# Optimization experiments

Measured on AMD Instinct MI355X. Metric: run time of the kernel, lower is better.

## Reference

```python
import jax, jax.numpy as jnp
import numpy as np

B, T, I, H, L = 64, 512, 512, 512, 2

def _xavier(key, shape):
    fan_in, fan_out = shape
    limit = float(np.sqrt(6.0 / (fan_in + fan_out)))
    return jax.random.uniform(key, shape, jnp.float32, -limit, limit)

def setup_inputs() -> dict:
    key = jax.random.key(0)
    ks = jax.random.split(key, 16)
    x = jax.random.normal(ks[0], (B, T, I), jnp.float32)
    h = jax.random.normal(ks[1], (L, B, H), jnp.float32)
    c = jax.random.normal(ks[2], (L, B, H), jnp.float32)
    # Gate order: i, f, g, o (concatenated along output dim -> [*, 4H])
    W_x0 = jnp.concatenate([_xavier(ks[3 + j], (I, H)) for j in range(4)], axis=1)
    W_h0 = jnp.concatenate([_xavier(ks[7 + j], (H, H)) for j in range(4)], axis=1)
    W_x1 = jnp.concatenate([_xavier(ks[11], (H, H)), _xavier(ks[12], (H, H)),
                            _xavier(ks[13], (H, H)), _xavier(ks[14], (H, H))], axis=1)
    W_h1 = jnp.concatenate([jax.random.split(ks[15], 4)[j] is None or _xavier(jax.random.split(ks[15], 4)[j], (H, H)) for j in range(4)], axis=1)
    # 8 scalar biases per layer: (b_ii, b_hi, b_if, b_hf, b_ig, b_hg, b_io, b_ho); zero-init as in torch
    b0 = jnp.zeros((8,), jnp.float32)
    b1 = jnp.zeros((8,), jnp.float32)
    return {"x": x, "h": h, "c": c, "W_x0": W_x0, "W_h0": W_h0, "b0": b0,
            "W_x1": W_x1, "W_h1": W_h1, "b1": b1}

def _lstm_layer(xs, h0, c0, Wx, Wh, b):
    # xs: [B, T, D]; Wx: [D, 4H]; Wh: [H, 4H]; b: [8] scalars
    bg = b[0::2] + b[1::2]  # combined per-gate scalar biases [4]: i, f, g, o
    x_proj = jnp.einsum('btd,dk->btk', xs, Wx)  # precompute input GEMM: [B, T, 4H]

    def step(carry, xp_t):
        h, c = carry
        z = xp_t + h @ Wh  # [B, 4H]
        zi, zf, zg, zo = jnp.split(z, 4, axis=1)
        i = jax.nn.sigmoid(zi + bg[0])
        f = jax.nn.sigmoid(zf + bg[1])
        g = jnp.tanh(zg + bg[2])
        o = jax.nn.sigmoid(zo + bg[3])
        c_new = f * c + i * g
        h_new = o * jnp.tanh(c_new)
        return (h_new, c_new), h_new

    (hT, cT), ys = jax.lax.scan(step, (h0, c0), jnp.swapaxes(x_proj, 0, 1))
    return jnp.swapaxes(ys, 0, 1), hT, cT  # output [B, T, H]

def reference(x, h, c, W_x0, W_h0, b0, W_x1, W_h1, b1):
    out0, h0T, c0T = _lstm_layer(x, h[0], c[0], W_x0, W_h0, b0)
    out1, h1T, c1T = _lstm_layer(out0, h[1], c[1], W_x1, W_h1, b1)
    new_h = jnp.stack([h0T, h1T])  # [L, B, H]
    new_c = jnp.stack([c0T, c1T])
    return out1, new_h, new_c
```

## Files before the change

kernel.cpp:

```cpp
#include <hip/hip_runtime.h>
#include <hip/hip_bf16.h>

#define B_   64
#define T_   512
#define I_   512
#define H_   512
#define NTHR 256

typedef short bf16x8 __attribute__((ext_vector_type(8)));
typedef float f32x4  __attribute__((ext_vector_type(4)));
typedef unsigned long long u64;
typedef unsigned short u16;

#define MFMA(a, b, c) __builtin_amdgcn_mfma_f32_16x16x32_bf16((a), (b), (c), 0, 0, 0)

__device__ __forceinline__ u16 f2b(float f) {
    __hip_bfloat16 h = __float2bfloat16(f);
    return __builtin_bit_cast(u16, h);
}

__device__ __forceinline__ u64 coh_ld64(const void* p) {
    return __hip_atomic_load((const u64*)p, __ATOMIC_RELAXED, __HIP_MEMORY_SCOPE_AGENT);
}
__device__ __forceinline__ void coh_st64(void* p, u64 v) {
    __hip_atomic_store((u64*)p, v, __ATOMIC_RELAXED, __HIP_MEMORY_SCOPE_AGENT);
}
__device__ __forceinline__ bool flag_ge(const int* f, int idx, int tgt) {
    return __hip_atomic_load(f + idx, __ATOMIC_RELAXED, __HIP_MEMORY_SCOPE_AGENT) >= tgt;
}

__device__ __forceinline__ int sc0_ld_i32(const int* p) {
    int v;
    asm volatile("global_load_dword %0, %1, off sc0\n\ts_waitcnt vmcnt(0)"
                 : "=&v"(v) : "v"(p) : "memory");
    return v;
}
__device__ __forceinline__ void sc0_st_i32(int* p, int v) {
    asm volatile("global_store_dword %0, %1, off sc0" :: "v"(p), "v"(v) : "memory");
}

#define GLD16(O, A)                                                         \
  asm volatile(                                                             \
    "global_load_dwordx4 %0, %16, off sc0\n\t"                              \
    "global_load_dwordx4 %1, %16, off offset:64 sc0\n\t"                    \
    "global_load_dwordx4 %2, %16, off offset:128 sc0\n\t"                   \
    "global_load_dwordx4 %3, %16, off offset:192 sc0\n\t"                   \
    "global_load_dwordx4 %4, %16, off offset:256 sc0\n\t"                   \
    "global_load_dwordx4 %5, %16, off offset:320 sc0\n\t"                   \
    "global_load_dwordx4 %6, %16, off offset:384 sc0\n\t"                   \
    "global_load_dwordx4 %7, %16, off offset:448 sc0\n\t"                   \
    "global_load_dwordx4 %8, %16, off offset:512 sc0\n\t"                   \
    "global_load_dwordx4 %9, %16, off offset:576 sc0\n\t"                   \
    "global_load_dwordx4 %10, %16, off offset:640 sc0\n\t"                  \
    "global_load_dwordx4 %11, %16, off offset:704 sc0\n\t"                  \
    "global_load_dwordx4 %12, %16, off offset:768 sc0\n\t"                  \
    "global_load_dwordx4 %13, %16, off offset:832 sc0\n\t"                  \
    "global_load_dwordx4 %14, %16, off offset:896 sc0\n\t"                  \
    "global_load_dwordx4 %15, %16, off offset:960 sc0\n\t"                  \
    "s_waitcnt vmcnt(0)"                                                    \
    : "=&v"(O[0]), "=&v"(O[1]), "=&v"(O[2]), "=&v"(O[3]),                   \
      "=&v"(O[4]), "=&v"(O[5]), "=&v"(O[6]), "=&v"(O[7]),                   \
      "=&v"(O[8]), "=&v"(O[9]), "=&v"(O[10]), "=&v"(O[11]),                 \
      "=&v"(O[12]), "=&v"(O[13]), "=&v"(O[14]), "=&v"(O[15])                \
    : "v"(A) : "memory")

__device__ __forceinline__ void pub_local(u16* ring, int* fp, int fval,
                                          const u16* sca, int lane, int U0) {
    const int r0 = lane >> 3, s0 = lane & 7;
    const int r1 = 8 + r0;
    u64 q0 = *(const u64*)(sca + r0 * 36 + s0 * 4);
    u64 q1 = *(const u64*)(sca + r1 * 36 + s0 * 4);
    u16* d0 = ring + r0 * 512 + U0 + s0 * 4;
    u16* d1 = ring + r1 * 512 + U0 + s0 * 4;
    asm volatile(
        "global_store_dwordx2 %0, %2, off sc0\n\t"
        "global_store_dwordx2 %1, %3, off sc0\n\t"
        "s_waitcnt vmcnt(0)"
        :: "v"(d0), "v"(d1), "v"(q0), "v"(q1) : "memory");
    if (lane == 0) sc0_st_i32(fp, fval);
}

__device__ __forceinline__ void pub_agent(u16* ring, int* fp, int fval,
                                          const u16* sca, int lane, int R0, int U0) {
    const int r0 = lane >> 3, s0 = lane & 7;
    const int r1 = 8 + r0;
    u64 q0 = *(const u64*)(sca + r0 * 36 + s0 * 4);
    u64 q1 = *(const u64*)(sca + r1 * 36 + s0 * 4);
    coh_st64(ring + (size_t)(R0 + r0) * 512 + U0 + s0 * 4, q0);
    coh_st64(ring + (size_t)(R0 + r1) * 512 + U0 + s0 * 4, q1);
    asm volatile("s_waitcnt vmcnt(0)" ::: "memory");
    if (lane == 0)
        __hip_atomic_store(fp, fval, __ATOMIC_RELAXED, __HIP_MEMORY_SCOPE_AGENT);
}

__global__ void k_init(const float* __restrict__ x, u16* __restrict__ xb,
                       int* __restrict__ fl) {
    long i = (long)blockIdx.x * 256 + threadIdx.x;
    if (i < 2097152) {
        const float* p = x + i * 8;
        float4 a = *(const float4*)p;
        float4 b = *(const float4*)(p + 4);
        union { u16 s[8]; bf16x8 v; } u;
        u.s[0]=f2b(a.x); u.s[1]=f2b(a.y); u.s[2]=f2b(a.z); u.s[3]=f2b(a.w);
        u.s[4]=f2b(b.x); u.s[5]=f2b(b.y); u.s[6]=f2b(b.z); u.s[7]=f2b(b.w);
        *(bf16x8*)(xb + i * 8) = u.v;
    } else if (i < 2097152 + 1024) {
        fl[i - 2097152] = -1;
    }
}

__global__ __launch_bounds__(NTHR, 1) void k_lstm(
    const u16* __restrict__ xb,
    const float* __restrict__ Wx0, const float* __restrict__ Wh0, const float* __restrict__ b0,
    const float* __restrict__ Wx1, const float* __restrict__ Wh1, const float* __restrict__ b1,
    const float* __restrict__ c_in, const float* __restrict__ h_in,
    u16* __restrict__ h0ag, u16* __restrict__ h1ag,
    u16* __restrict__ h0loc, u16* __restrict__ h1loc,
    int* __restrict__ f0ag, int* __restrict__ f1ag,
    int* __restrict__ f0loc, int* __restrict__ f1loc,
    int* __restrict__ xcc_tab, int* __restrict__ probe, int* __restrict__ verd,
    float* __restrict__ out)
{
    const int bid = blockIdx.x;
    if ((bid & 7) >= 4) return;
    const int g   = bid & 7;
    const int jj  = bid >> 3;
    const int lay = jj >> 4;
    const int u   = jj & 15;
    const int tid  = threadIdx.x;
    const int wave = tid >> 6;
    const int lane = tid & 63;
    const int n    = lane & 15;
    const int quad = lane >> 4;
    const int R0   = g * 16;
    const int U0   = u * 32;

    __shared__ __align__(16) u16   hstage[2][8192];
    __shared__ __align__(16) u16   sc_all[16 * 36];
    __shared__ __align__(16) float sc_h [4][16][8];
    __shared__ int s_local;
    __shared__ int s_ver;

    int myxcc;
    asm volatile("s_getreg_b32 %0, hwreg(HW_REG_XCC_ID)" : "=s"(myxcc));
    if (tid == 0)
        __hip_atomic_store(xcc_tab + bid, myxcc, __ATOMIC_RELAXED, __HIP_MEMORY_SCOPE_AGENT);

    const float* Wx = lay ? Wx1 : Wx0;
    const float* Wh = lay ? Wh1 : Wh0;
    const float* bb = lay ? b1  : b0;
    const float bi = bb[0] + bb[1];
    const float bf = bb[2] + bb[3];
    const float bg = bb[4] + bb[5];
    const float bo = bb[6] + bb[7];

    bf16x8 breg[2][32];
    #pragma unroll
    for (int ct = 0; ct < 2; ++ct) {
        const int gate = ct * 2 + (n >> 3);
        const int gcol = gate * 512 + U0 + wave * 8 + (n & 7);
        #pragma unroll
        for (int f = 0; f < 32; ++f) {
            const int kbase = f * 32 + quad * 8;
            bf16x8 w;
            #pragma unroll
            for (int j = 0; j < 8; ++j) {
                const int k = kbase + j;
                const float v = (k < 512) ? Wx[(size_t)k * 2048 + gcol]
                                          : Wh[(size_t)(k - 512) * 2048 + gcol];
                w[j] = (short)f2b(v);
            }
            breg[ct][f] = w;
        }
    }

    float creg[4];
    if (n < 8) {
        #pragma unroll
        for (int r = 0; r < 4; ++r)
            creg[r] = c_in[(size_t)lay * 32768
                           + (size_t)(R0 + quad * 4 + r) * 512 + U0 + wave * 8 + n];
    }

    if (wave == 0) {
        const int member = (lane & 31) * 8 + g;
        int v;
        for (;;) {
            v = __hip_atomic_load(xcc_tab + member, __ATOMIC_RELAXED, __HIP_MEMORY_SCOPE_AGENT);
            if (__all(v != -1)) break;
            __builtin_amdgcn_s_sleep(8);
        }
        const int v0 = __shfl(v, 0);
        if (lane == 0) s_local = __all(v == v0) ? 1 : 0;
    }
    __syncthreads();

    int myver = 0;
    if (s_local) {
        if (tid == 0) sc0_st_i32(probe + bid, 0x5a5a0000 | bid);
        if (wave == 0) {
            const int member = (lane & 31) * 8 + g;
            const int want = 0x5a5a0000 | member;
            int ok = 0;
            for (int it = 0; it < 4000 && !ok; ++it)
                ok = __all(sc0_ld_i32(probe + member) == want) ? 1 : 0;
            if (lane == 0) s_ver = ok;
        }
        __syncthreads();
        myver = s_ver;
    }

    if (tid == 0)
        __hip_atomic_store(verd + bid, myver, __ATOMIC_RELAXED, __HIP_MEMORY_SCOPE_AGENT);
    if (wave == 0) {
        const int member = (lane & 31) * 8 + g;
        int v;
        for (;;) {
            v = __hip_atomic_load(verd + member, __ATOMIC_RELAXED, __HIP_MEMORY_SCOPE_AGENT);
            if (__all(v != -1)) break;
            __builtin_amdgcn_s_sleep(8);
        }
        if (lane == 0) s_local = __all(v == 1) ? 1 : 0;
    }
    __syncthreads();
    const bool loc = (s_local != 0);

    if (n < 8) {
        #pragma unroll
        for (int r = 0; r < 4; ++r) {
            const int row = quad * 4 + r;
            const float hv = h_in[(size_t)lay * 32768
                                  + (size_t)(R0 + row) * 512 + U0 + wave * 8 + n];
            sc_all[row * 36 + wave * 8 + n] = f2b(hv);
        }
    }
    __syncthreads();
    if (loc) {
        if (wave == 3)
            pub_local((lay ? h1loc : h0loc) + (size_t)g * 65536 + 7 * 8192,
                      (lay ? f1loc : f0loc) + g * 16 + u, 0, sc_all, lane, U0);
    } else {
        if (wave == 0)
            pub_agent((lay ? h1ag : h0ag) + (size_t)7 * 32768,
                      (lay ? f1ag : f0ag) + g * 16 + u, 0, sc_all, lane, R0, U0);
    }

    const int fidx = g * 16 + n;

    if (loc) {
        int* pp0 = f0loc + g * 16 + n;
        int* pp1 = f1loc + g * 16 + n;
        if (lay == 0) {
            for (int t = 0; t < 512; ++t) {
                f32x4 acc0 = {0.f,0.f,0.f,0.f}, acc1 = {0.f,0.f,0.f,0.f};
                const u16* px = xb + ((size_t)(R0 + n) * T_ + t) * I_;
                bf16x8 xa[16];
                #pragma unroll
                for (int f = 0; f < 16; ++f) xa[f] = *(const bf16x8*)(px + f * 32 + quad * 8);
                #pragma unroll
                for (int f = 0; f < 16; ++f) {
                    acc0 = MFMA(xa[f], breg[0][f], acc0);
                    acc1 = MFMA(xa[f], breg[1][f], acc1);
                }
                if ((t & 3) == 0) {
                    for (;;) {
                        int a_ = sc0_ld_i32(pp0);
                        int b_ = sc0_ld_i32(pp1);
                        if (__all(a_ >= t && b_ >= t - 4)) break;
                    }
                } else {
                    while (!__all(sc0_ld_i32(pp0) >= t)) {}
                }
                const u16* ha = h0loc + (size_t)g * 65536
                                + (size_t)((t - 1) & 7) * 8192 + n * 512 + quad * 8;
                bf16x8 hf[16];
                GLD16(hf, ha);
                #pragma unroll
                for (int f = 0; f < 16; ++f) {
                    acc0 = MFMA(hf[f], breg[0][16 + f], acc0);
                    acc1 = MFMA(hf[f], breg[1][16 + f], acc1);
                }
                f32x4 x0, x1;
                #pragma unroll
                for (int r = 0; r < 4; ++r) {
                    x0[r] = __shfl_xor(acc0[r], 8);
                    x1[r] = __shfl_xor(acc1[r], 8);
                }
                if (n < 8) {
                    #pragma unroll
                    for (int r = 0; r < 4; ++r) {
                        const int row = quad * 4 + r;
                        const float zi = acc0[r] + bi, zf = x0[r] + bf;
                        const float zg = acc1[r] + bg, zo = x1[r] + bo;
                        const float ig = 1.f / (1.f + __expf(-zi));
                        const float fg = 1.f / (1.f + __expf(-zf));
                        const float gg = tanhf(zg);
                        const float og = 1.f / (1.f + __expf(-zo));
                        const float cn = fg * creg[r] + ig * gg;
                        const float hn = og * tanhf(cn);
                        creg[r] = cn;
                        sc_all[row * 36 + wave * 8 + n] = f2b(hn);
                        sc_h[wave][row][n] = hn;
                    }
                }
                __syncthreads();
                if (wave == (t & 3))
                    pub_local(h0loc + (size_t)g * 65536 + (size_t)(t & 7) * 8192,
                              f0loc + g * 16 + u, t + 1, sc_all, lane, U0);
                if (t == 511 && n < 8) {
                    const size_t o1 = (size_t)B_ * T_ * H_;
                    #pragma unroll
                    for (int r = 0; r < 4; ++r) {
                        const int grow = R0 + quad * 4 + r;
                        out[o1 + (size_t)grow * 512 + U0 + wave * 8 + n]
                            = sc_h[wave][quad * 4 + r][n];
                        out[o1 + 65536 + (size_t)grow * 512 + U0 + wave * 8 + n] = creg[r];
                    }
                }
            }
        } else {
            for (int t = 0; t < 512; ++t) {
                for (;;) {
                    int a_ = sc0_ld_i32(pp1);
                    int b_ = sc0_ld_i32(pp0);
                    if (__all(a_ >= t && b_ >= t + 1)) break;
                }
                const u16* a0p = h0loc + (size_t)g * 65536
                                 + (size_t)(t & 7) * 8192 + n * 512 + quad * 8;
                const u16* a1p = h1loc + (size_t)g * 65536
                                 + (size_t)((t - 1) & 7) * 8192 + n * 512 + quad * 8;
                f32x4 acc0 = {0.f,0.f,0.f,0.f}, acc1 = {0.f,0.f,0.f,0.f};
                bf16x8 hf[16];
                GLD16(hf, a0p);
                #pragma unroll
                for (int f = 0; f < 16; ++f) {
                    acc0 = MFMA(hf[f], breg[0][f], acc0);
                    acc1 = MFMA(hf[f], breg[1][f], acc1);
                }
                GLD16(hf, a1p);
                #pragma unroll
                for (int f = 0; f < 16; ++f) {
                    acc0 = MFMA(hf[f], breg[0][16 + f], acc0);
                    acc1 = MFMA(hf[f], breg[1][16 + f], acc1);
                }
                f32x4 x0, x1;
                #pragma unroll
                for (int r = 0; r < 4; ++r) {
                    x0[r] = __shfl_xor(acc0[r], 8);
                    x1[r] = __shfl_xor(acc1[r], 8);
                }
                if (n < 8) {
                    #pragma unroll
                    for (int r = 0; r < 4; ++r) {
                        const int row = quad * 4 + r;
                        const float zi = acc0[r] + bi, zf = x0[r] + bf;
                        const float zg = acc1[r] + bg, zo = x1[r] + bo;
                        const float ig = 1.f / (1.f + __expf(-zi));
                        const float fg = 1.f / (1.f + __expf(-zf));
                        const float gg = tanhf(zg);
                        const float og = 1.f / (1.f + __expf(-zo));
                        const float cn = fg * creg[r] + ig * gg;
                        const float hn = og * tanhf(cn);
                        creg[r] = cn;
                        sc_all[row * 36 + wave * 8 + n] = f2b(hn);
                        sc_h[wave][row][n] = hn;
                    }
                }
                __syncthreads();
                if (wave == (t & 3))
                    pub_local(h1loc + (size_t)g * 65536 + (size_t)(t & 7) * 8192,
                              f1loc + g * 16 + u, t + 1, sc_all, lane, U0);
                if (lane < 16) {
                    const float* s = &sc_h[wave][lane][0];
                    f32x4 a  = *(const f32x4*)s;
                    f32x4 b2 = *(const f32x4*)(s + 4);
                    float* po = out + ((size_t)(R0 + lane) * T_ + t) * H_ + U0 + wave * 8;
                    *(f32x4*)po       = a;
                    *(f32x4*)(po + 4) = b2;
                }
                if (t == 511 && n < 8) {
                    const size_t o1 = (size_t)B_ * T_ * H_;
                    #pragma unroll
                    for (int r = 0; r < 4; ++r) {
                        const int grow = R0 + quad * 4 + r;
                        out[o1 + 32768 + (size_t)grow * 512 + U0 + wave * 8 + n]
                            = sc_h[wave][quad * 4 + r][n];
                        out[o1 + 65536 + 32768 + (size_t)grow * 512 + U0 + wave * 8 + n]
                            = creg[r];
                    }
                }
            }
        }
        return;
    }

    for (int t = 0; t < 512; ++t) {
        f32x4 acc0 = {0.f,0.f,0.f,0.f}, acc1 = {0.f,0.f,0.f,0.f};
        if (lay == 0) {
            const u16* px = xb + ((size_t)(R0 + n) * T_ + t) * I_;
            bf16x8 xa[16];
            #pragma unroll
            for (int f = 0; f < 16; ++f) xa[f] = *(const bf16x8*)(px + f * 32 + quad * 8);
            #pragma unroll
            for (int f = 0; f < 16; ++f) {
                acc0 = MFMA(xa[f], breg[0][f], acc0);
                acc1 = MFMA(xa[f], breg[1][f], acc1);
            }
            const bool bp = (t & 3) == 0;
            for (;;) {
                bool ok = flag_ge(f0ag, fidx, t);
                if (bp) ok = ok && flag_ge(f1ag, fidx, t - 4);
                if (__all(ok)) break;
                __builtin_amdgcn_s_sleep(1);
            }
            asm volatile("" ::: "memory");
            const u16* base = h0ag + (size_t)((t - 1) & 7) * 32768;
            u64 v[8];
            #pragma unroll
            for (int i = 0; i < 8; ++i) {
                const int s = i * 256 + tid;
                const int r = s >> 7, m = s & 127;
                v[i] = coh_ld64(base + (size_t)(R0 + r) * 512 + m * 4);
            }
            #pragma unroll
            for (int i = 0; i < 8; ++i) {
                const int s = i * 256 + tid;
                const int r = s >> 7, m = s & 127;
                const int uu = m >> 1, sub = m & 1;
                *(u64*)&hstage[0][r * 512 + (((uu ^ (r & 7)) << 3) | (sub << 2))] = v[i];
            }
            __syncthreads();
            #pragma unroll
            for (int f = 0; f < 16; ++f) {
                bf16x8 ha = *(const bf16x8*)
                    &hstage[0][n * 512 + (((f * 4 + quad) ^ (n & 7)) << 3)];
                acc0 = MFMA(ha, breg[0][16 + f], acc0);
                acc1 = MFMA(ha, breg[1][16 + f], acc1);
            }
        } else {
            for (;;) {
                bool ok = flag_ge(f1ag, fidx, t) && flag_ge(f0ag, fidx, t + 1);
                if (__all(ok)) break;
                __builtin_amdgcn_s_sleep(1);
            }
            asm volatile("" ::: "memory");
            const u16* base0 = h0ag + (size_t)(t & 7) * 32768;
            const u16* base1 = h1ag + (size_t)((t - 1) & 7) * 32768;
            u64 v0[8], v1[8];
            #pragma unroll
            for (int i = 0; i < 8; ++i) {
                const int s = i * 256 + tid;
                const int r = s >> 7, m = s & 127;
                v0[i] = coh_ld64(base0 + (size_t)(R0 + r) * 512 + m * 4);
                v1[i] = coh_ld64(base1 + (size_t)(R0 + r) * 512 + m * 4);
            }
            #pragma unroll
            for (int i = 0; i < 8; ++i) {
                const int s = i * 256 + tid;
                const int r = s >> 7, m = s & 127;
                const int uu = m >> 1, sub = m & 1;
                const int off = r * 512 + (((uu ^ (r & 7)) << 3) | (sub << 2));
                *(u64*)&hstage[0][off] = v0[i];
                *(u64*)&hstage[1][off] = v1[i];
            }
            __syncthreads();
            #pragma unroll
            for (int f = 0; f < 16; ++f) {
                const int off = n * 512 + (((f * 4 + quad) ^ (n & 7)) << 3);
                bf16x8 ha = *(const bf16x8*)&hstage[0][off];
                acc0 = MFMA(ha, breg[0][f], acc0);
                acc1 = MFMA(ha, breg[1][f], acc1);
                bf16x8 hb = *(const bf16x8*)&hstage[1][off];
                acc0 = MFMA(hb, breg[0][16 + f], acc0);
                acc1 = MFMA(hb, breg[1][16 + f], acc1);
            }
        }
        f32x4 x0, x1;
        #pragma unroll
        for (int r = 0; r < 4; ++r) {
            x0[r] = __shfl_xor(acc0[r], 8);
            x1[r] = __shfl_xor(acc1[r], 8);
        }
        if (n < 8) {
            #pragma unroll
            for (int r = 0; r < 4; ++r) {
                const int row = quad * 4 + r;
                const float zi = acc0[r] + bi, zf = x0[r] + bf;
                const float zg = acc1[r] + bg, zo = x1[r] + bo;
                const float ig = 1.f / (1.f + __expf(-zi));
                const float fg = 1.f / (1.f + __expf(-zf));
                const float gg = tanhf(zg);
                const float og = 1.f / (1.f + __expf(-zo));
                const float cn = fg * creg[r] + ig * gg;
                const float hn = og * tanhf(cn);
                creg[r] = cn;
                sc_all[row * 36 + wave * 8 + n] = f2b(hn);
                sc_h[wave][row][n] = hn;
            }
        }
        __syncthreads();
        if (wave == 0)
            pub_agent((lay ? h1ag : h0ag) + (size_t)(t & 7) * 32768,
                      (lay ? f1ag : f0ag) + g * 16 + u, t + 1, sc_all, lane, R0, U0);
        if (lay && lane < 16) {
            const float* s = &sc_h[wave][lane][0];
            f32x4 a  = *(const f32x4*)s;
            f32x4 b2 = *(const f32x4*)(s + 4);
            float* po = out + ((size_t)(R0 + lane) * T_ + t) * H_ + U0 + wave * 8;
            *(f32x4*)po       = a;
            *(f32x4*)(po + 4) = b2;
        }
        if (t == 511 && n < 8) {
            const size_t o1 = (size_t)B_ * T_ * H_;
            #pragma unroll
            for (int r = 0; r < 4; ++r) {
                const int grow = R0 + quad * 4 + r;
                out[o1 + (size_t)lay * 32768 + (size_t)grow * 512 + U0 + wave * 8 + n]
                    = sc_h[wave][quad * 4 + r][n];
                out[o1 + 65536 + (size_t)lay * 32768 + (size_t)grow * 512 + U0 + wave * 8 + n]
                    = creg[r];
            }
        }
    }
}

extern "C" void kernel_launch(void* const* d_in, const int* in_sizes, int n_in,
                              void* d_out, int out_size, void* d_ws, size_t ws_size,
                              hipStream_t stream) {
    const float* x   = (const float*)d_in[0];
    const float* h   = (const float*)d_in[1];
    const float* c   = (const float*)d_in[2];
    const float* Wx0 = (const float*)d_in[3];
    const float* Wh0 = (const float*)d_in[4];
    const float* b0  = (const float*)d_in[5];
    const float* Wx1 = (const float*)d_in[6];
    const float* Wh1 = (const float*)d_in[7];
    const float* b1  = (const float*)d_in[8];
    float* out = (float*)d_out;

    u16* xb     = (u16*)d_ws;
    u16* h0ag   = xb + 16777216;
    u16* h1ag   = h0ag + 262144;
    u16* h0loc  = h1ag + 262144;
    u16* h1loc  = h0loc + 262144;
    int* f0ag   = (int*)(h1loc + 262144);
    int* f1ag   = f0ag + 64;
    int* f0loc  = f1ag + 64;
    int* f1loc  = f0loc + 64;
    int* xcc    = f1loc + 64;
    int* probe  = xcc + 256;
    int* verd   = probe + 256;

    k_init<<<8196, 256, 0, stream>>>(x, xb, f0ag);
    k_lstm<<<256, NTHR, 0, stream>>>(xb, Wx0, Wh0, b0, Wx1, Wh1, b1, c, h,
                                     h0ag, h1ag, h0loc, h1loc,
                                     f0ag, f1ag, f0loc, f1loc, xcc, probe, verd, out);
}
```

Measured before the change: 2.938 ms.

## Use per-wave flags and direct stores in local LSTM path, drop block barrier

In the same-XCC (local) path, each wave now publishes its own slice of h directly to the ring and sets its own flag, replacing the per-step __syncthreads plus single-wave publish. Consumers poll 64 per-wave flags with one lane each. The flag arrays are enlarged and their init extended to match. Gate activations switch to exp2/rcp intrinsic approximations in place of expf/tanhf. The intent is to remove the block-wide barrier and the serialized publish from the recurrent critical path, at the cost of more flag traffic and slightly lower activation accuracy.

```diff
diff --git a/kernel.cpp b/kernel.cpp
--- a/kernel.cpp
+++ b/kernel.cpp
@@ -19,6 +19,15 @@
     return __builtin_bit_cast(u16, h);
 }
 
+__device__ __forceinline__ float fsig(float x) {
+    float e = __builtin_amdgcn_exp2f(-1.442695040888963f * x);
+    return __builtin_amdgcn_rcpf(1.f + e);
+}
+__device__ __forceinline__ float ftanh(float x) {
+    float e = __builtin_amdgcn_exp2f(2.885390081777927f * x);
+    return 1.f - 2.f * __builtin_amdgcn_rcpf(e + 1.f);
+}
+
 __device__ __forceinline__ u64 coh_ld64(const void* p) {
     return __hip_atomic_load((const u64*)p, __ATOMIC_RELAXED, __HIP_MEMORY_SCOPE_AGENT);
 }
@@ -37,6 +46,9 @@
 }
 __device__ __forceinline__ void sc0_st_i32(int* p, int v) {
     asm volatile("global_store_dword %0, %1, off sc0" :: "v"(p), "v"(v) : "memory");
+}
+__device__ __forceinline__ void sc0_st128(void* p, bf16x8 v) {
+    asm volatile("global_store_dwordx4 %0, %1, off sc0" :: "v"(p), "v"(v) : "memory");
 }
 
 #define GLD16(O, A)                                                         \
@@ -64,22 +76,6 @@
       "=&v"(O[12]), "=&v"(O[13]), "=&v"(O[14]), "=&v"(O[15])                \
     : "v"(A) : "memory")
 
-__device__ __forceinline__ void pub_local(u16* ring, int* fp, int fval,
-                                          const u16* sca, int lane, int U0) {
-    const int r0 = lane >> 3, s0 = lane & 7;
-    const int r1 = 8 + r0;
-    u64 q0 = *(const u64*)(sca + r0 * 36 + s0 * 4);
-    u64 q1 = *(const u64*)(sca + r1 * 36 + s0 * 4);
-    u16* d0 = ring + r0 * 512 + U0 + s0 * 4;
-    u16* d1 = ring + r1 * 512 + U0 + s0 * 4;
-    asm volatile(
-        "global_store_dwordx2 %0, %2, off sc0\n\t"
-        "global_store_dwordx2 %1, %3, off sc0\n\t"
-        "s_waitcnt vmcnt(0)"
-        :: "v"(d0), "v"(d1), "v"(q0), "v"(q1) : "memory");
-    if (lane == 0) sc0_st_i32(fp, fval);
-}
-
 __device__ __forceinline__ void pub_agent(u16* ring, int* fp, int fval,
                                           const u16* sca, int lane, int R0, int U0) {
     const int r0 = lane >> 3, s0 = lane & 7;
@@ -104,7 +100,7 @@
         u.s[0]=f2b(a.x); u.s[1]=f2b(a.y); u.s[2]=f2b(a.z); u.s[3]=f2b(a.w);
         u.s[4]=f2b(b.x); u.s[5]=f2b(b.y); u.s[6]=f2b(b.z); u.s[7]=f2b(b.w);
         *(bf16x8*)(xb + i * 8) = u.v;
-    } else if (i < 2097152 + 1024) {
+    } else if (i < 2097152 + 1408) {
         fl[i - 2097152] = -1;
     }
 }
@@ -137,7 +133,8 @@
 
     __shared__ __align__(16) u16   hstage[2][8192];
     __shared__ __align__(16) u16   sc_all[16 * 36];
-    __shared__ __align__(16) float sc_h [4][16][8];
+    __shared__ __align__(16) u16   swb [4][16][8];
+    __shared__ __align__(16) float sc_h[4][16][8];
     __shared__ int s_local;
     __shared__ int s_ver;
 
@@ -225,6 +222,122 @@
     __syncthreads();
     const bool loc = (s_local != 0);
 
+    const int fidx = g * 16 + n;
+
+    if (loc) {
+        int* fl0 = f0loc + g * 64;
+        int* fl1 = f1loc + g * 64;
+        int* myf = (lay ? fl1 : fl0) + u * 4 + wave;
+        const int* p0 = fl0 + lane;
+        const int* p1 = fl1 + lane;
+        u16* ring  = (lay ? h1loc : h0loc) + (size_t)g * 65536;
+        u16* ring0 = h0loc + (size_t)g * 65536;
+        u16* ring1 = h1loc + (size_t)g * 65536;
+
+        if (lane < 16) {
+            const float* hp = h_in + (size_t)lay * 32768
+                              + (size_t)(R0 + lane) * 512 + U0 + wave * 8;
+            union { u16 s[8]; bf16x8 v; } pk;
+            #pragma unroll
+            for (int j = 0; j < 8; ++j) pk.s[j] = f2b(hp[j]);
+            sc0_st128(ring + 7 * 8192 + lane * 512 + U0 + wave * 8, pk.v);
+        }
+        asm volatile("s_waitcnt vmcnt(0)" ::: "memory");
+        if (lane == 0) sc0_st_i32(myf, 0);
+
+        for (int t = 0; t < 512; ++t) {
+            f32x4 acc0 = {0.f,0.f,0.f,0.f}, acc1 = {0.f,0.f,0.f,0.f};
+            bf16x8 hf[16];
+
+            if (lay == 0) {
+                const u16* px = xb + ((size_t)(R0 + n) * T_ + t) * I_;
+                bf16x8 xa[16];
+                #pragma unroll
+                for (int f = 0; f < 16; ++f) xa[f] = *(const bf16x8*)(px + f * 32 + quad * 8);
+                #pragma unroll
+                for (int f = 0; f < 16; ++f) {
+                    acc0 = MFMA(xa[f], breg[0][f], acc0);
+                    acc1 = MFMA(xa[f], breg[1][f], acc1);
+                }
+                if ((t & 3) == 0)
+                    while (!__all(sc0_ld_i32(p1) >= t - 4)) {}
+                while (!__all(sc0_ld_i32(p0) >= t)) {}
+                GLD16(hf, ring0 + (size_t)((t - 1) & 7) * 8192 + n * 512 + quad * 8);
+                #pragma unroll
+                for (int f = 0; f < 16; ++f) {
+                    acc0 = MFMA(hf[f], breg[0][16 + f], acc0);
+                    acc1 = MFMA(hf[f], breg[1][16 + f], acc1);
+                }
+            } else {
+                while (!__all(sc0_ld_i32(p0) >= t + 1)) {}
+                GLD16(hf, ring0 + (size_t)(t & 7) * 8192 + n * 512 + quad * 8);
+                #pragma unroll
+                for (int f = 0; f < 16; ++f) {
+                    acc0 = MFMA(hf[f], breg[0][f], acc0);
+                    acc1 = MFMA(hf[f], breg[1][f], acc1);
+                }
+                while (!__all(sc0_ld_i32(p1) >= t)) {}
+                GLD16(hf, ring1 + (size_t)((t - 1) & 7) * 8192 + n * 512 + quad * 8);
+                #pragma unroll
+                for (int f = 0; f < 16; ++f) {
+                    acc0 = MFMA(hf[f], breg[0][16 + f], acc0);
+                    acc1 = MFMA(hf[f], breg[1][16 + f], acc1);
+                }
+            }
+
+            f32x4 x0, x1;
+            #pragma unroll
+            for (int r = 0; r < 4; ++r) {
+                x0[r] = __shfl_xor(acc0[r], 8);
+                x1[r] = __shfl_xor(acc1[r], 8);
+            }
+            if (n < 8) {
+                #pragma unroll
+                for (int r = 0; r < 4; ++r) {
+                    const int row = quad * 4 + r;
+                    const float ig = fsig(acc0[r] + bi);
+                    const float fg = fsig(x0[r]   + bf);
+                    const float gg = ftanh(acc1[r] + bg);
+                    const float og = fsig(x1[r]   + bo);
+                    const float cn = fg * creg[r] + ig * gg;
+                    const float hn = og * ftanh(cn);
+                    creg[r] = cn;
+                    swb [wave][row][n] = f2b(hn);
+                    sc_h[wave][row][n] = hn;
+                }
+            }
+            asm volatile("s_waitcnt lgkmcnt(0)" ::: "memory");
+            __builtin_amdgcn_sched_barrier(0);
+            if (lane < 16) {
+                bf16x8 hv = *(const bf16x8*)&swb[wave][lane][0];
+                sc0_st128(ring + (size_t)(t & 7) * 8192 + lane * 512 + U0 + wave * 8, hv);
+            }
+            asm volatile("s_waitcnt vmcnt(0)" ::: "memory");
+            if (lane == 0) sc0_st_i32(myf, t + 1);
+
+            if (lay && lane < 16) {
+                const float* s = &sc_h[wave][lane][0];
+                f32x4 a  = *(const f32x4*)s;
+                f32x4 b2 = *(const f32x4*)(s + 4);
+                float* po = out + ((size_t)(R0 + lane) * T_ + t) * H_ + U0 + wave * 8;
+                *(f32x4*)po       = a;
+                *(f32x4*)(po + 4) = b2;
+            }
+            if (t == 511 && n < 8) {
+                const size_t o1 = (size_t)B_ * T_ * H_;
+                #pragma unroll
+                for (int r = 0; r < 4; ++r) {
+                    const int grow = R0 + quad * 4 + r;
+                    out[o1 + (size_t)lay * 32768 + (size_t)grow * 512 + U0 + wave * 8 + n]
+                        = sc_h[wave][quad * 4 + r][n];
+                    out[o1 + 65536 + (size_t)lay * 32768 + (size_t)grow * 512 + U0 + wave * 8 + n]
+                        = creg[r];
+                }
+            }
+        }
+        return;
+    }
+
     if (n < 8) {
         #pragma unroll
         for (int r = 0; r < 4; ++r) {
@@ -235,164 +348,9 @@
         }
     }
     __syncthreads();
-    if (loc) {
-        if (wave == 3)
-            pub_local((lay ? h1loc : h0loc) + (size_t)g * 65536 + 7 * 8192,
-                      (lay ? f1loc : f0loc) + g * 16 + u, 0, sc_all, lane, U0);
-    } else {
-        if (wave == 0)
-            pub_agent((lay ? h1ag : h0ag) + (size_t)7 * 32768,
-                      (lay ? f1ag : f0ag) + g * 16 + u, 0, sc_all, lane, R0, U0);
-    }
-
-    const int fidx = g * 16 + n;
-
-    if (loc) {
-        int* pp0 = f0loc + g * 16 + n;
-        int* pp1 = f1loc + g * 16 + n;
-        if (lay == 0) {
-            for (int t = 0; t < 512; ++t) {
-                f32x4 acc0 = {0.f,0.f,0.f,0.f}, acc1 = {0.f,0.f,0.f,0.f};
-                const u16* px = xb + ((size_t)(R0 + n) * T_ + t) * I_;
-                bf16x8 xa[16];
-                #pragma unroll
-                for (int f = 0; f < 16; ++f) xa[f] = *(const bf16x8*)(px + f * 32 + quad * 8);
-                #pragma unroll
-                for (int f = 0; f < 16; ++f) {
-                    acc0 = MFMA(xa[f], breg[0][f], acc0);
-                    acc1 = MFMA(xa[f], breg[1][f], acc1);
-                }
-                if ((t & 3) == 0) {
-                    for (;;) {
-                        int a_ = sc0_ld_i32(pp0);
-                        int b_ = sc0_ld_i32(pp1);
-                        if (__all(a_ >= t && b_ >= t - 4)) break;
-                    }
-                } else {
-                    while (!__all(sc0_ld_i32(pp0) >= t)) {}
-                }
-                const u16* ha = h0loc + (size_t)g * 65536
-                                + (size_t)((t - 1) & 7) * 8192 + n * 512 + quad * 8;
-                bf16x8 hf[16];
-                GLD16(hf, ha);
-                #pragma unroll
-                for (int f = 0; f < 16; ++f) {
-                    acc0 = MFMA(hf[f], breg[0][16 + f], acc0);
-                    acc1 = MFMA(hf[f], breg[1][16 + f], acc1);
-                }
-                f32x4 x0, x1;
-                #pragma unroll
-                for (int r = 0; r < 4; ++r) {
-                    x0[r] = __shfl_xor(acc0[r], 8);
-                    x1[r] = __shfl_xor(acc1[r], 8);
-                }
-                if (n < 8) {
-                    #pragma unroll
-                    for (int r = 0; r < 4; ++r) {
-                        const int row = quad * 4 + r;
-                        const float zi = acc0[r] + bi, zf = x0[r] + bf;
-                        const float zg = acc1[r] + bg, zo = x1[r] + bo;
-                        const float ig = 1.f / (1.f + __expf(-zi));
-                        const float fg = 1.f / (1.f + __expf(-zf));
-                        const float gg = tanhf(zg);
-                        const float og = 1.f / (1.f + __expf(-zo));
-                        const float cn = fg * creg[r] + ig * gg;
-                        const float hn = og * tanhf(cn);
-                        creg[r] = cn;
-                        sc_all[row * 36 + wave * 8 + n] = f2b(hn);
-                        sc_h[wave][row][n] = hn;
-                    }
-                }
-                __syncthreads();
-                if (wave == (t & 3))
-                    pub_local(h0loc + (size_t)g * 65536 + (size_t)(t & 7) * 8192,
-                              f0loc + g * 16 + u, t + 1, sc_all, lane, U0);
-                if (t == 511 && n < 8) {
-                    const size_t o1 = (size_t)B_ * T_ * H_;
-                    #pragma unroll
-                    for (int r = 0; r < 4; ++r) {
-                        const int grow = R0 + quad * 4 + r;
-                        out[o1 + (size_t)grow * 512 + U0 + wave * 8 + n]
-                            = sc_h[wave][quad * 4 + r][n];
-                        out[o1 + 65536 + (size_t)grow * 512 + U0 + wave * 8 + n] = creg[r];
-                    }
-                }
-            }
-        } else {
-            for (int t = 0; t < 512; ++t) {
-                for (;;) {
-                    int a_ = sc0_ld_i32(pp1);
-                    int b_ = sc0_ld_i32(pp0);
-                    if (__all(a_ >= t && b_ >= t + 1)) break;
-                }
-                const u16* a0p = h0loc + (size_t)g * 65536
-                                 + (size_t)(t & 7) * 8192 + n * 512 + quad * 8;
-                const u16* a1p = h1loc + (size_t)g * 65536
-                                 + (size_t)((t - 1) & 7) * 8192 + n * 512 + quad * 8;
-                f32x4 acc0 = {0.f,0.f,0.f,0.f}, acc1 = {0.f,0.f,0.f,0.f};
-                bf16x8 hf[16];
-                GLD16(hf, a0p);
-                #pragma unroll
-                for (int f = 0; f < 16; ++f) {
-                    acc0 = MFMA(hf[f], breg[0][f], acc0);
-                    acc1 = MFMA(hf[f], breg[1][f], acc1);
-                }
-                GLD16(hf, a1p);
-                #pragma unroll
-                for (int f = 0; f < 16; ++f) {
-                    acc0 = MFMA(hf[f], breg[0][16 + f], acc0);
-                    acc1 = MFMA(hf[f], breg[1][16 + f], acc1);
-                }
-                f32x4 x0, x1;
-                #pragma unroll
-                for (int r = 0; r < 4; ++r) {
-                    x0[r] = __shfl_xor(acc0[r], 8);
-                    x1[r] = __shfl_xor(acc1[r], 8);
-                }
-                if (n < 8) {
-                    #pragma unroll
-                    for (int r = 0; r < 4; ++r) {
-                        const int row = quad * 4 + r;
-                        const float zi = acc0[r] + bi, zf = x0[r] + bf;
-                        const float zg = acc1[r] + bg, zo = x1[r] + bo;
-                        const float ig = 1.f / (1.f + __expf(-zi));
-                        const float fg = 1.f / (1.f + __expf(-zf));
-                        const float gg = tanhf(zg);
-                        const float og = 1.f / (1.f + __expf(-zo));
-                        const float cn = fg * creg[r] + ig * gg;
-                        const float hn = og * tanhf(cn);
-                        creg[r] = cn;
-                        sc_all[row * 36 + wave * 8 + n] = f2b(hn);
-                        sc_h[wave][row][n] = hn;
-                    }
-                }
-                __syncthreads();
-                if (wave == (t & 3))
-                    pub_local(h1loc + (size_t)g * 65536 + (size_t)(t & 7) * 8192,
-                              f1loc + g * 16 + u, t + 1, sc_all, lane, U0);
-                if (lane < 16) {
-                    const float* s = &sc_h[wave][lane][0];
-                    f32x4 a  = *(const f32x4*)s;
-                    f32x4 b2 = *(const f32x4*)(s + 4);
-                    float* po = out + ((size_t)(R0 + lane) * T_ + t) * H_ + U0 + wave * 8;
-                    *(f32x4*)po       = a;
-                    *(f32x4*)(po + 4) = b2;
-                }
-                if (t == 511 && n < 8) {
-                    const size_t o1 = (size_t)B_ * T_ * H_;
-                    #pragma unroll
-                    for (int r = 0; r < 4; ++r) {
-                        const int grow = R0 + quad * 4 + r;
-                        out[o1 + 32768 + (size_t)grow * 512 + U0 + wave * 8 + n]
-                            = sc_h[wave][quad * 4 + r][n];
-                        out[o1 + 65536 + 32768 + (size_t)grow * 512 + U0 + wave * 8 + n]
-                            = creg[r];
-                    }
-                }
-            }
-        }
-        return;
-    }
+    if (wave == 0)
+        pub_agent((lay ? h1ag : h0ag) + (size_t)7 * 32768,
+                  (lay ? f1ag : f0ag) + g * 16 + u, 0, sc_all, lane, R0, U0);
 
     for (int t = 0; t < 512; ++t) {
         f32x4 acc0 = {0.f,0.f,0.f,0.f}, acc1 = {0.f,0.f,0.f,0.f};
@@ -546,12 +504,12 @@
     int* f0ag   = (int*)(h1loc + 262144);
     int* f1ag   = f0ag + 64;
     int* f0loc  = f1ag + 64;
-    int* f1loc  = f0loc + 64;
-    int* xcc    = f1loc + 64;
+    int* f1loc  = f0loc + 256;
+    int* xcc    = f1loc + 256;
     int* probe  = xcc + 256;
     int* verd   = probe + 256;
 
-    k_init<<<8196, 256, 0, stream>>>(x, xb, f0ag);
+    k_init<<<8198, 256, 0, stream>>>(x, xb, f0ag);
     k_lstm<<<256, NTHR, 0, stream>>>(xb, Wx0, Wh0, b0, Wx1, Wh1, b1, c, h,
                                      h0ag, h1ag, h0loc, h1loc,
                                      f0ag, f1ag, f0loc, f1loc, xcc, probe, verd, out);
```

New measurement: 2.984 ms. About the same (+1.6%).
